# Kernel optimization log

Hardware: AMD Instinct MI355X
Metric: run time of the kernel (lower is better)

## Reference

```python
import jax, jax.numpy as jnp
import numpy as np

N_NODES = 18870
HIDDEN = 256
K = 20
HEAD_HIDDEN = 512
N_CLASSES = 3
N_GENES_OUT = 6640
B = 1024
FALLBACK_SCALE = 1e-3
LN_EPS = 1e-5


def setup_inputs() -> dict:
    key = jax.random.key(0)
    ks = jax.random.split(key, 8)
    node_idx = jax.random.randint(ks[0], (B,), 0, N_NODES)
    topk_neighbors = jax.random.randint(ks[1], (N_NODES, K), 0, N_NODES)
    node_emb = jax.random.normal(ks[2], (N_NODES, HIDDEN), dtype=jnp.float32)
    fallback_emb = jax.random.normal(ks[3], (HIDDEN,), dtype=jnp.float32) * 0.02
    w_attn = jax.random.normal(ks[4], (HIDDEN,), dtype=jnp.float32) * 0.02
    ln_gamma = jnp.ones((2 * HIDDEN,), dtype=jnp.float32)
    ln_beta = jnp.zeros((2 * HIDDEN,), dtype=jnp.float32)
    W1 = jax.random.normal(ks[5], (2 * HIDDEN, HEAD_HIDDEN), dtype=jnp.float32) * 0.02
    b1 = jnp.zeros((HEAD_HIDDEN,), dtype=jnp.float32)
    W2 = jax.random.normal(ks[6], (HEAD_HIDDEN, N_CLASSES * N_GENES_OUT), dtype=jnp.float32) * 0.02
    b2 = jnp.zeros((N_CLASSES * N_GENES_OUT,), dtype=jnp.float32)
    return dict(node_idx=node_idx, topk_neighbors=topk_neighbors, node_emb=node_emb,
                fallback_emb=fallback_emb, w_attn=w_attn, ln_gamma=ln_gamma, ln_beta=ln_beta,
                W1=W1, b1=b1, W2=W2, b2=b2)


def reference(node_idx, topk_neighbors, node_emb, fallback_emb, w_attn,
              ln_gamma, ln_beta, W1, b1, W2, b2):
    valid = node_idx >= 0                                   # [B]
    safe_idx = jnp.where(valid, node_idx, 0)                # [B]
    graph_emb = node_emb[safe_idx]                          # [B, H]
    pert_emb = jnp.where(valid[:, None],
                         graph_emb + FALLBACK_SCALE * fallback_emb[None, :],
                         fallback_emb[None, :])              # [B, H]

    nbr_idx = topk_neighbors[safe_idx]                      # [B, K]
    valid_nbr = nbr_idx >= 0                                # [B, K]
    nbr_emb = node_emb[jnp.clip(nbr_idx, 0)]                # [B, K, H]
    nbr_emb = nbr_emb * valid_nbr[..., None].astype(nbr_emb.dtype)

    # Faithful to the original broadcast: scores[b,k] = pert_emb[b,0] * (nbr_emb[b,k] . w_attn)
    scores = pert_emb[:, 0:1] * jnp.einsum('bkh,h->bk', nbr_emb, w_attn)  # [B, K]
    scores = jnp.where(valid_nbr, scores, -1e9)
    has_valid = jnp.any(valid_nbr, axis=1, keepdims=True)   # [B, 1]
    attn = jnp.where(has_valid, jax.nn.softmax(scores, axis=-1),
                     jnp.zeros_like(scores))                # [B, K]
    context = jnp.einsum('bk,bkh->bh', attn, nbr_emb)       # [B, H]

    combined = jnp.concatenate([pert_emb, context], axis=-1)  # [B, 2H]
    mu = jnp.mean(combined, axis=-1, keepdims=True)
    var = jnp.mean(jnp.square(combined - mu), axis=-1, keepdims=True)
    x = (combined - mu) * jax.lax.rsqrt(var + LN_EPS) * ln_gamma + ln_beta
    h = jax.nn.gelu(x @ W1 + b1, approximate=False)          # [B, HH]
    logits = h @ W2 + b2                                     # [B, 3*6640]
    return logits.reshape(-1, N_CLASSES, N_GENES_OUT)


if __name__ == '__main__':
    out = reference(**setup_inputs())
    print(out.shape)
```

## Files before the change

### kernel.cpp

```cpp
#include <hip/hip_runtime.h>
#include <hip/hip_bf16.h>
#include <math.h>

#define HIDDEN 256
#define K_NBR 20
#define NB 1024

typedef __bf16 bf16x8 __attribute__((ext_vector_type(8)));
typedef float f32x4 __attribute__((ext_vector_type(4)));

__device__ __forceinline__ float wave_sum(float v) {
#pragma unroll
    for (int o = 32; o > 0; o >>= 1) v += __shfl_xor(v, o, 64);
    return v;
}

__device__ __forceinline__ void gload16(const void* g, void* l) {
    __builtin_amdgcn_global_load_lds(
        (const __attribute__((address_space(1))) void*)g,
        (__attribute__((address_space(3))) void*)l, 16, 0, 0);
}

__device__ __forceinline__ int swz3(int g, int row) {
    return (g & ~7) | ((g & 7) ^ (row & 7));
}
__device__ __forceinline__ int swz2(int g, int row) {
    return (g & ~3) | ((g & 3) ^ ((row >> 1) & 3));
}

__device__ __forceinline__ void attn_ln_body(
    int b, int t, const int* __restrict__ node_idx, const int* __restrict__ topk,
    const float* __restrict__ node_emb, const float* __restrict__ fallback,
    const float* __restrict__ w_attn, const float* __restrict__ gamma,
    const float* __restrict__ beta, __bf16* __restrict__ xb,
    float* pe, float (*nbr)[HIDDEN], int* nidx, float* sc, float* red)
{
    int lane = t & 63, w = t >> 6;
    int nid = node_idx[b];
    bool valid = nid >= 0;
    int safe = valid ? nid : 0;

    pe[t] = valid ? node_emb[(size_t)safe * HIDDEN + t] + 1e-3f * fallback[t]
                  : fallback[t];
    if (t < K_NBR) nidx[t] = topk[safe * K_NBR + t];
    __syncthreads();
    for (int r = 0; r < K_NBR; ++r) {
        int gi = nidx[r];
        nbr[r][t] = (gi >= 0) ? node_emb[(size_t)gi * HIDDEN + t] : 0.f;
    }
    __syncthreads();
    float pe0 = pe[0];
    float wa[4];
#pragma unroll
    for (int q = 0; q < 4; ++q) wa[q] = w_attn[lane + 64 * q];
    for (int k = w; k < K_NBR; k += 4) {
        float p = 0.f;
#pragma unroll
        for (int q = 0; q < 4; ++q) p += nbr[k][lane + 64 * q] * wa[q];
        p = wave_sum(p);
        if (lane == 0) sc[k] = (nidx[k] >= 0) ? pe0 * p : -1e9f;
    }
    __syncthreads();
    bool has_valid = false;
#pragma unroll
    for (int k = 0; k < K_NBR; ++k) has_valid |= (nidx[k] >= 0);
    float mx = -1e30f;
#pragma unroll
    for (int k = 0; k < K_NBR; ++k) mx = fmaxf(mx, sc[k]);
    float at[K_NBR];
    float s = 0.f;
#pragma unroll
    for (int k = 0; k < K_NBR; ++k) { at[k] = expf(sc[k] - mx); s += at[k]; }
    float inv = has_valid ? 1.f / s : 0.f;
    float ctx = 0.f;
#pragma unroll
    for (int k = 0; k < K_NBR; ++k) ctx += (at[k] * inv) * nbr[k][t];
    float v0 = pe[t], v1 = ctx;
    float s1 = wave_sum(v0 + v1);
    float s2 = wave_sum(v0 * v0 + v1 * v1);
    if (lane == 0) { red[w] = s1; red[4 + w] = s2; }
    __syncthreads();
    s1 = red[0] + red[1] + red[2] + red[3];
    s2 = red[4] + red[5] + red[6] + red[7];
    float mu = s1 / 512.f;
    float var = s2 / 512.f - mu * mu;
    float rs = rsqrtf(var + 1e-5f);
    size_t base = (size_t)b * 512;
    int mask = b & 7;
    {
        int e = t;
        int g = e >> 3, off = e & 7;
        int gp = (g & ~7) | ((g & 7) ^ mask);
        xb[base + gp * 8 + off] = (__bf16)((v0 - mu) * rs * gamma[t] + beta[t]);
        e = 256 + t;
        g = e >> 3;
        gp = (g & ~7) | ((g & 7) ^ mask);
        xb[base + gp * 8 + off] = (__bf16)((v1 - mu) * rs * gamma[256 + t] + beta[256 + t]);
    }
}

__device__ __forceinline__ void transpose_body(
    const float* __restrict__ Wm, __bf16* __restrict__ WT,
    int Kd, int Nd, int Np, int bx, int by, int t, int two_bit)
{
    int n = bx * 64 + (t >> 2);
    int k0 = by * 32 + (t & 3) * 8;
    bool ok = n < Nd;
    bf16x8 v;
#pragma unroll
    for (int j = 0; j < 8; ++j) {
        float f = ok ? Wm[(size_t)(k0 + j) * Nd + n] : 0.f;
        v[j] = (__bf16)f;
    }
    if (n < Np) {
        int g = k0 >> 3;
        int gp = two_bit ? swz2(g, n) : swz3(g, n);
        *(bf16x8*)(WT + (size_t)n * Kd + gp * 8) = v;
    }
}

__global__ __launch_bounds__(256) void prep_kernel(
    const int* __restrict__ node_idx, const int* __restrict__ topk,
    const float* __restrict__ node_emb, const float* __restrict__ fallback,
    const float* __restrict__ w_attn, const float* __restrict__ gamma,
    const float* __restrict__ beta, const float* __restrict__ W1,
    const float* __restrict__ W2, __bf16* __restrict__ xb,
    __bf16* __restrict__ w1t, __bf16* __restrict__ w2t)
{
    __shared__ float pe[HIDDEN];
    __shared__ float nbr[K_NBR][HIDDEN];
    __shared__ int   nidx[K_NBR];
    __shared__ float sc[K_NBR];
    __shared__ float red[8];
    int bid = blockIdx.x;
    int t = threadIdx.x;
    if (bid < 4992) { transpose_body(W2, w2t, 512, 19920, 19968, bid % 312, bid / 312, t, 1); return; }
    bid -= 4992;
    if (bid < 128) { transpose_body(W1, w1t, 512, 512, 512, bid % 8, bid / 8, t, 0); return; }
    bid -= 128;
    attn_ln_body(bid, t, node_idx, topk, node_emb, fallback, w_attn, gamma, beta,
                 xb, pe, nbr, nidx, sc, red);
}

__global__ __launch_bounds__(256, 4) void gemm1_kernel(
    const __bf16* __restrict__ A, const __bf16* __restrict__ BT,
    const float* __restrict__ bias, __bf16* __restrict__ Cb,
    int M, int N, int K)
{
    constexpr int BK = 64;
    __shared__ __bf16 As[2][64 * BK];
    __shared__ __bf16 Bs[2][64 * BK];

    int t = threadIdx.x;
    int lane = t & 63;
    int wid = t >> 6;
    int wm = wid >> 1, wn = wid & 1;
    int lo = lane & 15, hi = lane >> 4;

    int nwg = gridDim.x;
    int bid = blockIdx.x;
    int cpx = nwg >> 3;
    int lid = (bid & 7) * cpx + (bid >> 3);
    int m0 = (lid & 15) * 64;
    int n0 = (lid >> 4) * 64;

    int rsub = lane >> 3, kc = lane & 7;

    auto STAGE = [&](int buf, int k0) {
#pragma unroll
        for (int j = 0; j < 2; ++j) {
            int rb = j * 32 + wid * 8;
            gload16(A + (size_t)(m0 + rb + rsub) * K + k0 + kc * 8, &As[buf][rb * BK]);
        }
#pragma unroll
        for (int j = 0; j < 2; ++j) {
            int rb = j * 32 + wid * 8;
            gload16(BT + (size_t)(n0 + rb + rsub) * K + k0 + kc * 8, &Bs[buf][rb * BK]);
        }
    };

    f32x4 acc[2][2];
#pragma unroll
    for (int m = 0; m < 2; ++m)
#pragma unroll
        for (int n = 0; n < 2; ++n) acc[m][n] = (f32x4){0.f, 0.f, 0.f, 0.f};

    auto COMPUTE = [&](int buf) {
#pragma unroll
        for (int ks = 0; ks < 2; ++ks) {
            bf16x8 af[2], bfr[2];
#pragma unroll
            for (int m = 0; m < 2; ++m) {
                int r = wm * 32 + m * 16 + lo;
                af[m] = *(const bf16x8*)&As[buf][r * BK + (((ks * 4 + hi) ^ (r & 7)) * 8)];
            }
#pragma unroll
            for (int n = 0; n < 2; ++n) {
                int r = wn * 32 + n * 16 + lo;
                bfr[n] = *(const bf16x8*)&Bs[buf][r * BK + (((ks * 4 + hi) ^ (r & 7)) * 8)];
            }
#pragma unroll
            for (int m = 0; m < 2; ++m)
#pragma unroll
                for (int n = 0; n < 2; ++n)
                    acc[m][n] = __builtin_amdgcn_mfma_f32_16x16x32_bf16(
                        af[m], bfr[n], acc[m][n], 0, 0, 0);
        }
    };

    const int nt = K / BK;
    STAGE(0, 0);
    for (int tt = 0; tt < nt - 1; ++tt) {
        STAGE((tt + 1) & 1, (tt + 1) * BK);
        asm volatile("s_waitcnt vmcnt(4)" ::: "memory");
        __builtin_amdgcn_s_barrier();
        __builtin_amdgcn_sched_barrier(0);
        COMPUTE(tt & 1);
        __builtin_amdgcn_sched_barrier(0);
        __builtin_amdgcn_s_barrier();
    }
    asm volatile("s_waitcnt vmcnt(0)" ::: "memory");
    __builtin_amdgcn_s_barrier();
    __builtin_amdgcn_sched_barrier(0);
    COMPUTE((nt - 1) & 1);

#pragma unroll
    for (int m = 0; m < 2; ++m) {
        int gr = m0 + wm * 32 + m * 16 + hi * 4;
#pragma unroll
        for (int n = 0; n < 2; ++n) {
            int gc = n0 + wn * 32 + n * 16 + lo;
            float bv = bias[gc];
#pragma unroll
            for (int r = 0; r < 4; ++r) {
                float v = acc[m][n][r] + bv;
                float g = v * 0.5f * (1.f + erff(v * 0.70710678118f));
                int row = gr + r;
                int gp = swz2(gc >> 3, row);
                Cb[(size_t)row * N + gp * 8 + (gc & 7)] = (__bf16)g;
            }
        }
    }
}

__global__ __launch_bounds__(512, 8) void gemm2_kernel(
    const __bf16* __restrict__ A, const __bf16* __restrict__ BT,
    const float* __restrict__ bias, float* __restrict__ C,
    int M, int N, int K)
{
    constexpr int BK = 32;
    __shared__ __bf16 As[2][128 * BK];
    __shared__ __bf16 Bs[2][128 * BK];

    int t = threadIdx.x;
    int lane = t & 63;
    int wid = t >> 6;
    int wm = wid >> 2, wn = wid & 3;
    int lo = lane & 15, hi = lane >> 4;

    int nwg = gridDim.x;
    int bid = blockIdx.x;
    int cpx = nwg >> 3;
    int lid = (bid & 7) * cpx + (bid >> 3);
    int m0 = (lid & 7) * 128;
    int n0 = (lid >> 3) * 128;

    int srow = t >> 2;
    int ssl = t & 3;

    auto STAGE = [&](int buf, int tt) {
        int k0 = tt * BK;
        gload16(A + (size_t)(m0 + srow) * K + k0 + ssl * 8, &As[buf][wid * 512]);
        gload16(BT + (size_t)(n0 + srow) * K + k0 + ssl * 8, &Bs[buf][wid * 512]);
    };

    f32x4 acc[4][2];
#pragma unroll
    for (int m = 0; m < 4; ++m)
#pragma unroll
        for (int n = 0; n < 2; ++n) acc[m][n] = (f32x4){0.f, 0.f, 0.f, 0.f};

    auto COMPUTE = [&](int buf) {
        bf16x8 af[4], bfr[2];
#pragma unroll
        for (int m = 0; m < 4; ++m) {
            int r = wm * 64 + m * 16 + lo;
            af[m] = *(const bf16x8*)&As[buf][r * BK + ((hi ^ ((r >> 1) & 3)) * 8)];
        }
#pragma unroll
        for (int n = 0; n < 2; ++n) {
            int r = wn * 32 + n * 16 + lo;
            bfr[n] = *(const bf16x8*)&Bs[buf][r * BK + ((hi ^ ((r >> 1) & 3)) * 8)];
        }
#pragma unroll
        for (int m = 0; m < 4; ++m)
#pragma unroll
            for (int n = 0; n < 2; ++n)
                acc[m][n] = __builtin_amdgcn_mfma_f32_16x16x32_bf16(
                    af[m], bfr[n], acc[m][n], 0, 0, 0);
    };

    const int nt = K / BK;
    STAGE(0, 0);
    for (int tt = 0; tt < nt - 1; ++tt) {
        STAGE((tt + 1) & 1, tt + 1);
        asm volatile("s_waitcnt vmcnt(2)" ::: "memory");
        __builtin_amdgcn_s_barrier();
        __builtin_amdgcn_sched_barrier(0);
        COMPUTE(tt & 1);
        __builtin_amdgcn_sched_barrier(0);
        __builtin_amdgcn_s_barrier();
    }
    asm volatile("s_waitcnt vmcnt(0)" ::: "memory");
    __builtin_amdgcn_s_barrier();
    __builtin_amdgcn_sched_barrier(0);
    COMPUTE((nt - 1) & 1);

#pragma unroll
    for (int m = 0; m < 4; ++m) {
        int gr = m0 + wm * 64 + m * 16 + hi * 4;
#pragma unroll
        for (int n = 0; n < 2; ++n) {
            int gc = n0 + wn * 32 + n * 16 + lo;
            if (gc < N) {
                float bv = bias[gc];
#pragma unroll
                for (int r = 0; r < 4; ++r)
                    C[(size_t)(gr + r) * N + gc] = acc[m][n][r] + bv;
            }
        }
    }
}

extern "C" void kernel_launch(void* const* d_in, const int* in_sizes, int n_in,
                              void* d_out, int out_size, void* d_ws, size_t ws_size,
                              hipStream_t stream) {
    const int*   node_idx = (const int*)d_in[0];
    const int*   topk     = (const int*)d_in[1];
    const float* node_emb = (const float*)d_in[2];
    const float* fallback = (const float*)d_in[3];
    const float* w_attn   = (const float*)d_in[4];
    const float* gamma    = (const float*)d_in[5];
    const float* beta     = (const float*)d_in[6];
    const float* W1       = (const float*)d_in[7];
    const float* b1       = (const float*)d_in[8];
    const float* W2       = (const float*)d_in[9];
    const float* b2       = (const float*)d_in[10];
    float* out = (float*)d_out;

    const int M = 1024, Kd = 512, N1 = 512, N2 = 19920;
    const int N2p = 19968;

    __bf16* xb  = (__bf16*)d_ws;
    __bf16* h   = xb + (size_t)M * Kd;
    __bf16* w1t = h + (size_t)M * Kd;
    __bf16* w2t = w1t + (size_t)N1 * Kd;

    prep_kernel<<<4992 + 128 + 1024, 256, 0, stream>>>(
        node_idx, topk, node_emb, fallback, w_attn, gamma, beta, W1, W2,
        xb, w1t, w2t);

    gemm1_kernel<<<dim3(128), 256, 0, stream>>>(
        xb, w1t, b1, h, M, N1, Kd);

    gemm2_kernel<<<dim3(1248), 512, 0, stream>>>(
        h, w2t, b2, out, M, N2, Kd);
    (void)ws_size;
}
```

Measured before the change: 75.25 us.

## Retile gemm2 to 64x128 with BK=64 and reorder prep blocks

Changes the second GEMM tile from 128x128 with BK=32 to 64x128 with BK=64, doubling the grid to 2496 blocks and halving the MFMA work per wave. The LDS swizzle moves to an 8-way XOR pattern to match the wider K slice. In the same commit, the h and W2-transpose producers switch to that swizzle, and the prep kernel now schedules the attention/LN blocks before the weight transposes. The smaller M tile means more blocks for better occupancy and balance, at the cost of more reloads of W2 per output.

```diff
diff --git a/kernel.cpp b/kernel.cpp
--- a/kernel.cpp
+++ b/kernel.cpp
@@ -23,9 +23,6 @@
 
 __device__ __forceinline__ int swz3(int g, int row) {
     return (g & ~7) | ((g & 7) ^ (row & 7));
-}
-__device__ __forceinline__ int swz2(int g, int row) {
-    return (g & ~3) | ((g & 3) ^ ((row >> 1) & 3));
 }
 
 __device__ __forceinline__ void attn_ln_body(
@@ -101,7 +98,7 @@
 
 __device__ __forceinline__ void transpose_body(
     const float* __restrict__ Wm, __bf16* __restrict__ WT,
-    int Kd, int Nd, int Np, int bx, int by, int t, int two_bit)
+    int Kd, int Nd, int Np, int bx, int by, int t)
 {
     int n = bx * 64 + (t >> 2);
     int k0 = by * 32 + (t & 3) * 8;
@@ -113,8 +110,7 @@
         v[j] = (__bf16)f;
     }
     if (n < Np) {
-        int g = k0 >> 3;
-        int gp = two_bit ? swz2(g, n) : swz3(g, n);
+        int gp = swz3(k0 >> 3, n);
         *(bf16x8*)(WT + (size_t)n * Kd + gp * 8) = v;
     }
 }
@@ -134,12 +130,15 @@
     __shared__ float red[8];
     int bid = blockIdx.x;
     int t = threadIdx.x;
-    if (bid < 4992) { transpose_body(W2, w2t, 512, 19920, 19968, bid % 312, bid / 312, t, 1); return; }
-    bid -= 4992;
-    if (bid < 128) { transpose_body(W1, w1t, 512, 512, 512, bid % 8, bid / 8, t, 0); return; }
+    if (bid < 1024) {
+        attn_ln_body(bid, t, node_idx, topk, node_emb, fallback, w_attn, gamma,
+                     beta, xb, pe, nbr, nidx, sc, red);
+        return;
+    }
+    bid -= 1024;
+    if (bid < 128) { transpose_body(W1, w1t, 512, 512, 512, bid % 8, bid / 8, t); return; }
     bid -= 128;
-    attn_ln_body(bid, t, node_idx, topk, node_emb, fallback, w_attn, gamma, beta,
-                 xb, pe, nbr, nidx, sc, red);
+    transpose_body(W2, w2t, 512, 19920, 19968, bid % 312, bid / 312, t);
 }
 
 __global__ __launch_bounds__(256, 4) void gemm1_kernel(
@@ -236,20 +235,20 @@
                 float v = acc[m][n][r] + bv;
                 float g = v * 0.5f * (1.f + erff(v * 0.70710678118f));
                 int row = gr + r;
-                int gp = swz2(gc >> 3, row);
+                int gp = swz3(gc >> 3, row);
                 Cb[(size_t)row * N + gp * 8 + (gc & 7)] = (__bf16)g;
             }
         }
     }
 }
 
-__global__ __launch_bounds__(512, 8) void gemm2_kernel(
+__global__ __launch_bounds__(512, 6) void gemm2_kernel(
     const __bf16* __restrict__ A, const __bf16* __restrict__ BT,
     const float* __restrict__ bias, float* __restrict__ C,
     int M, int N, int K)
 {
-    constexpr int BK = 32;
-    __shared__ __bf16 As[2][128 * BK];
+    constexpr int BK = 64;
+    __shared__ __bf16 As[2][64 * BK];
     __shared__ __bf16 Bs[2][128 * BK];
 
     int t = threadIdx.x;
@@ -262,49 +261,55 @@
     int bid = blockIdx.x;
     int cpx = nwg >> 3;
     int lid = (bid & 7) * cpx + (bid >> 3);
-    int m0 = (lid & 7) * 128;
-    int n0 = (lid >> 3) * 128;
-
-    int srow = t >> 2;
-    int ssl = t & 3;
-
-    auto STAGE = [&](int buf, int tt) {
-        int k0 = tt * BK;
-        gload16(A + (size_t)(m0 + srow) * K + k0 + ssl * 8, &As[buf][wid * 512]);
-        gload16(BT + (size_t)(n0 + srow) * K + k0 + ssl * 8, &Bs[buf][wid * 512]);
+    int m0 = (lid & 15) * 64;
+    int n0 = (lid >> 4) * 128;
+
+    int rsub = lane >> 3, kc = lane & 7;
+
+    auto STAGE = [&](int buf, int k0) {
+        gload16(A + (size_t)(m0 + wid * 8 + rsub) * K + k0 + kc * 8,
+                &As[buf][(wid * 8) * BK]);
+#pragma unroll
+        for (int j = 0; j < 2; ++j) {
+            int rb = j * 64 + wid * 8;
+            gload16(BT + (size_t)(n0 + rb + rsub) * K + k0 + kc * 8, &Bs[buf][rb * BK]);
+        }
     };
 
-    f32x4 acc[4][2];
-#pragma unroll
-    for (int m = 0; m < 4; ++m)
+    f32x4 acc[2][2];
+#pragma unroll
+    for (int m = 0; m < 2; ++m)
 #pragma unroll
         for (int n = 0; n < 2; ++n) acc[m][n] = (f32x4){0.f, 0.f, 0.f, 0.f};
 
     auto COMPUTE = [&](int buf) {
-        bf16x8 af[4], bfr[2];
-#pragma unroll
-        for (int m = 0; m < 4; ++m) {
-            int r = wm * 64 + m * 16 + lo;
-            af[m] = *(const bf16x8*)&As[buf][r * BK + ((hi ^ ((r >> 1) & 3)) * 8)];
-        }
-#pragma unroll
-        for (int n = 0; n < 2; ++n) {
-            int r = wn * 32 + n * 16 + lo;
-            bfr[n] = *(const bf16x8*)&Bs[buf][r * BK + ((hi ^ ((r >> 1) & 3)) * 8)];
-        }
-#pragma unroll
-        for (int m = 0; m < 4; ++m)
-#pragma unroll
-            for (int n = 0; n < 2; ++n)
-                acc[m][n] = __builtin_amdgcn_mfma_f32_16x16x32_bf16(
-                    af[m], bfr[n], acc[m][n], 0, 0, 0);
+#pragma unroll
+        for (int ks = 0; ks < 2; ++ks) {
+            bf16x8 af[2], bfr[2];
+#pragma unroll
+            for (int m = 0; m < 2; ++m) {
+                int r = wm * 32 + m * 16 + lo;
+                af[m] = *(const bf16x8*)&As[buf][r * BK + (((ks * 4 + hi) ^ (r & 7)) * 8)];
+            }
+#pragma unroll
+            for (int n = 0; n < 2; ++n) {
+                int r = wn * 32 + n * 16 + lo;
+                bfr[n] = *(const bf16x8*)&Bs[buf][r * BK + (((ks * 4 + hi) ^ (r & 7)) * 8)];
+            }
+#pragma unroll
+            for (int m = 0; m < 2; ++m)
+#pragma unroll
+                for (int n = 0; n < 2; ++n)
+                    acc[m][n] = __builtin_amdgcn_mfma_f32_16x16x32_bf16(
+                        af[m], bfr[n], acc[m][n], 0, 0, 0);
+        }
     };
 
     const int nt = K / BK;
     STAGE(0, 0);
     for (int tt = 0; tt < nt - 1; ++tt) {
-        STAGE((tt + 1) & 1, tt + 1);
-        asm volatile("s_waitcnt vmcnt(2)" ::: "memory");
+        STAGE((tt + 1) & 1, (tt + 1) * BK);
+        asm volatile("s_waitcnt vmcnt(3)" ::: "memory");
         __builtin_amdgcn_s_barrier();
         __builtin_amdgcn_sched_barrier(0);
         COMPUTE(tt & 1);
@@ -317,8 +322,8 @@
     COMPUTE((nt - 1) & 1);
 
 #pragma unroll
-    for (int m = 0; m < 4; ++m) {
-        int gr = m0 + wm * 64 + m * 16 + hi * 4;
+    for (int m = 0; m < 2; ++m) {
+        int gr = m0 + wm * 32 + m * 16 + hi * 4;
 #pragma unroll
         for (int n = 0; n < 2; ++n) {
             int gc = n0 + wn * 32 + n * 16 + lo;
@@ -349,21 +354,20 @@
     float* out = (float*)d_out;
 
     const int M = 1024, Kd = 512, N1 = 512, N2 = 19920;
-    const int N2p = 19968;
 
     __bf16* xb  = (__bf16*)d_ws;
     __bf16* h   = xb + (size_t)M * Kd;
     __bf16* w1t = h + (size_t)M * Kd;
     __bf16* w2t = w1t + (size_t)N1 * Kd;
 
-    prep_kernel<<<4992 + 128 + 1024, 256, 0, stream>>>(
+    prep_kernel<<<1024 + 128 + 4992, 256, 0, stream>>>(
         node_idx, topk, node_emb, fallback, w_attn, gamma, beta, W1, W2,
         xb, w1t, w2t);
 
     gemm1_kernel<<<dim3(128), 256, 0, stream>>>(
         xb, w1t, b1, h, M, N1, Kd);
 
-    gemm2_kernel<<<dim3(1248), 512, 0, stream>>>(
+    gemm2_kernel<<<dim3(2496), 512, 0, stream>>>(
         h, w2t, b2, out, M, N2, Kd);
     (void)ws_size;
 }
```

Measured after the change: 69.23 us (median of 2 runs). -8.0%, faster.
